# Kernel optimization log

Measured on AMD Instinct MI355X. Metric: run time of the kernel, lower is better.

The kernel has to match this reference:

```python
import jax, jax.numpy as jnp
import numpy as np

DIM_X, H1, H2 = 1024, 2048, 512
SL, SU = 8192, 16384
K_TRIES = 8  # vectorized stand-in for the per-sample rejection-sampling while-loop


def setup_inputs() -> dict:
    key = jax.random.key(0)
    ks = jax.random.split(key, 10)
    s = 0.02
    return {
        "X_l": jax.random.normal(ks[0], (SL, DIM_X), jnp.float32),
        "y_l": jax.random.normal(ks[1], (SL,), jnp.float32),
        "X_u": jax.random.normal(ks[2], (SU, DIM_X), jnp.float32),
        "y_u": jax.random.normal(ks[3], (SU,), jnp.float32),
        "W1": jax.random.normal(ks[4], (DIM_X, H1), jnp.float32) * s,
        "b1": jnp.zeros((H1,), jnp.float32),
        "W2": jax.random.normal(ks[5], (H1, H2), jnp.float32) * s,
        "b2": jnp.zeros((H2,), jnp.float32),
        "W3": jax.random.normal(ks[6], (H2, 1), jnp.float32) * s,
        "b3": jnp.zeros((1,), jnp.float32),
    }


def _sample_pairs(key, y_l, size_u):
    """For each unlabeled sample, draw a labeled pair (a, b) with a != b and
    y_l[a] != y_l[b] (mirrors torch.randperm + rejection loop). K candidate
    draws per sample; first valid candidate is taken (valid w.h.p. for
    continuous y_l)."""
    size_l = y_l.shape[0]
    ka, kb = jax.random.split(key)
    ia = jax.random.randint(ka, (size_u, K_TRIES), 0, size_l)  # [SU, K]
    ib = jax.random.randint(kb, (size_u, K_TRIES), 0, size_l)
    valid = (ia != ib) & (y_l[ia] != y_l[ib])
    first = jnp.argmax(valid, axis=1)  # first valid candidate per row
    a = jnp.take_along_axis(ia, first[:, None], axis=1)[:, 0]
    b = jnp.take_along_axis(ib, first[:, None], axis=1)[:, 0]
    return a, b


def reference(X_l, y_l, X_u, y_u, W1, b1, W2, b2, W3, b3):
    def encode(x):
        h = jax.nn.relu(x @ W1 + b1)
        return jax.nn.relu(h @ W2 + b2)

    feat_l = encode(X_l)          # [SL, H2]
    feat_u = encode(X_u)          # [SU, H2]
    y_hat = feat_l @ W3 + b3      # [SL, 1]

    a, b = _sample_pairs(jax.random.key(42), y_l, X_u.shape[0])
    k = (y_u - y_l[b]) / (y_l[a] - y_l[b])            # [SU]
    feat_comb = k[:, None] * feat_l[a] + (1.0 - k)[:, None] * feat_l[b]
    return feat_u, feat_comb, y_hat
```

## Files before the change

kernel.cpp:

```cpp
#include <hip/hip_runtime.h>
#include <stdint.h>

#define SLAB 8192
#define SUNL 16384
#define DIMX 1024
#define HID1 2048
#define HID2 512
#define KTRIES 8
#define MTOT (SLAB + SUNL)

typedef __attribute__((ext_vector_type(8))) short bf16x8;
typedef __attribute__((ext_vector_type(4))) float f32x4;

__device__ __forceinline__ unsigned short f2bf(float f) {
  union { float f; uint32_t u; } c; c.f = f;
  return (unsigned short)((c.u + 0x7fffu + ((c.u >> 16) & 1u)) >> 16);
}

__device__ __forceinline__ void async16(const void* g, void* l) {
  __builtin_amdgcn_global_load_lds(
      (const __attribute__((address_space(1))) unsigned int*)g,
      (__attribute__((address_space(3))) unsigned int*)l,
      16, 0, 0);
}

struct U2 { uint32_t x, y; };

__device__ __forceinline__ U2 threefry(uint32_t k0, uint32_t k1, uint32_t x0, uint32_t x1) {
  uint32_t ks2 = k0 ^ k1 ^ 0x1BD11BDAu;
  x0 += k0; x1 += k1;
#define TF_R(r) { x0 += x1; x1 = (x1 << (r)) | (x1 >> (32 - (r))); x1 ^= x0; }
  TF_R(13) TF_R(15) TF_R(26) TF_R(6)
  x0 += k1; x1 += ks2 + 1u;
  TF_R(17) TF_R(29) TF_R(16) TF_R(24)
  x0 += ks2; x1 += k0 + 2u;
  TF_R(13) TF_R(15) TF_R(26) TF_R(6)
  x0 += k0; x1 += k1 + 3u;
  TF_R(17) TF_R(29) TF_R(16) TF_R(24)
  x0 += k1; x1 += ks2 + 4u;
  TF_R(13) TF_R(15) TF_R(26) TF_R(6)
  x0 += ks2; x1 += k0 + 5u;
#undef TF_R
  return {x0, x1};
}

#define XL_BLOCKS (SLAB * DIMX / 4 / 256)
#define CAST_BLOCKS (MTOT * DIMX / 4 / 256)
#define T1_NBX (HID1 / 32)
#define T1_BLOCKS ((HID1 / 32) * (DIMX / 32))
#define T2_NBX (HID2 / 32)
#define T2_BLOCKS ((HID2 / 32) * (HID1 / 32))
#define PAIR_BLOCKS (SUNL / 256)
#define PREP_BLOCKS (CAST_BLOCKS + T1_BLOCKS + T2_BLOCKS + PAIR_BLOCKS)

__global__ __launch_bounds__(256) void prep_kernel(
    const float* __restrict__ Xl, const float* __restrict__ Xu,
    const float* __restrict__ W1, const float* __restrict__ W2,
    const float* __restrict__ y_l, const float* __restrict__ y_u,
    unsigned short* __restrict__ X_bf, unsigned short* __restrict__ W1T,
    unsigned short* __restrict__ W2T,
    int* __restrict__ ia, int* __restrict__ ib, float* __restrict__ kv)
{
  __shared__ float t[32][33];
  int b = blockIdx.x;
  int tid = threadIdx.x;

  if (b < CAST_BLOCKS) {
    const float* src; size_t i, doff;
    if (b < XL_BLOCKS) { src = Xl; i = (size_t)b * 256 + tid; doff = 0; }
    else { src = Xu; i = (size_t)(b - XL_BLOCKS) * 256 + tid; doff = (size_t)SLAB * DIMX / 4; }
    float4 v = ((const float4*)src)[i];
    ushort4 o;
    o.x = f2bf(v.x); o.y = f2bf(v.y); o.z = f2bf(v.z); o.w = f2bf(v.w);
    ((ushort4*)X_bf)[doff + i] = o;
  } else if (b < CAST_BLOCKS + T1_BLOCKS + T2_BLOCKS) {
    const float* W; unsigned short* WT; int K, N, bx, by;
    if (b < CAST_BLOCKS + T1_BLOCKS) {
      int tb = b - CAST_BLOCKS;
      W = W1; WT = W1T; K = DIMX; N = HID1; bx = tb % T1_NBX; by = tb / T1_NBX;
    } else {
      int tb = b - CAST_BLOCKS - T1_BLOCKS;
      W = W2; WT = W2T; K = HID1; N = HID2; bx = tb % T2_NBX; by = tb / T2_NBX;
    }
    int k0 = by * 32, n0 = bx * 32;
    int tx = tid & 31, ty = tid >> 5;
#pragma unroll
    for (int i = 0; i < 32; i += 8)
      t[ty + i][tx] = W[(size_t)(k0 + ty + i) * N + n0 + tx];
    __syncthreads();
#pragma unroll
    for (int i = 0; i < 32; i += 8)
      WT[(size_t)(n0 + ty + i) * K + k0 + tx] = f2bf(t[tx][ty + i]);
  } else {
    int r = (b - CAST_BLOCKS - T1_BLOCKS - T2_BLOCKS) * 256 + tid;
    U2 ka  = threefry(0u, 42u, 0u, 0u);
    U2 kb  = threefry(0u, 42u, 0u, 1u);
    U2 k2a = threefry(ka.x, ka.y, 0u, 1u);
    U2 k2b = threefry(kb.x, kb.y, 0u, 1u);
    int iav[KTRIES], ibv[KTRIES];
#pragma unroll
    for (int c = 0; c < KTRIES; ++c) {
      uint32_t tt = (uint32_t)(r * KTRIES + c);
      U2 oa = threefry(k2a.x, k2a.y, 0u, tt);
      U2 ob = threefry(k2b.x, k2b.y, 0u, tt);
      iav[c] = (int)((oa.x ^ oa.y) & (SLAB - 1));
      ibv[c] = (int)((ob.x ^ ob.y) & (SLAB - 1));
    }
    int a = iav[0], bb2 = ibv[0];
#pragma unroll
    for (int c = 0; c < KTRIES; ++c) {
      if (iav[c] != ibv[c] && y_l[iav[c]] != y_l[ibv[c]]) { a = iav[c]; bb2 = ibv[c]; break; }
    }
    float ya = y_l[a], yb = y_l[bb2];
    ia[r] = a; ib[r] = bb2; kv[r] = (y_u[r] - yb) / (ya - yb);
  }
}

#define GROUP_M 8
#define MFMA_B16(a, b, c) __builtin_amdgcn_mfma_f32_16x16x32_bf16(a, b, c, 0, 0, 0)
#define SBAR __builtin_amdgcn_sched_barrier(0)

template<bool QP, bool ST, int VMC, bool BARS, bool PRE>
__device__ __forceinline__ void ktile32(
    const unsigned short* AsB, const unsigned short* BsB,
    unsigned short* AsS, unsigned short* BsS,
    const unsigned short* AsN, const unsigned short* BsN,
    const unsigned short* gA0, const unsigned short* gA1,
    const unsigned short* gB0, const unsigned short* gB1,
    int kk2, int ldstA, int ofsA, int ofsB,
    bf16x8 (&ha0)[4], bf16x8 (&hb0)[2],
    bf16x8 (&na0)[4], bf16x8 (&nb0)[2],
    bf16x8 (&ca1)[4], bf16x8 (&cb1)[2],
    bf16x8 (&ta1)[4], bf16x8 (&tb1)[2],
    f32x4 (&acc)[8][4])
{
#pragma unroll
  for (int j = 0; j < 2; ++j)
    tb1[j] = *(const bf16x8*)(BsB + ofsB + (j + 2) * 512);
  SBAR;
  if (QP) {
    __builtin_amdgcn_s_setprio(1);
#pragma unroll
    for (int i = 0; i < 4; ++i)
#pragma unroll
      for (int j = 0; j < 2; ++j)
        acc[i + 4][j + 2] = MFMA_B16(ca1[i], cb1[j], acc[i + 4][j + 2]);
    __builtin_amdgcn_s_setprio(0);
    SBAR;
  }
  asm volatile("s_waitcnt lgkmcnt(2)" ::: "memory");
  SBAR;
  __builtin_amdgcn_s_setprio(1);
#pragma unroll
  for (int i = 0; i < 4; ++i)
#pragma unroll
    for (int j = 0; j < 2; ++j)
      acc[i][j] = MFMA_B16(ha0[i], hb0[j], acc[i][j]);
  __builtin_amdgcn_s_setprio(0);
  SBAR;

#pragma unroll
  for (int i = 0; i < 4; ++i)
    ta1[i] = *(const bf16x8*)(AsB + ofsA + (i + 4) * 512);
  SBAR;
  asm volatile("s_waitcnt lgkmcnt(4)" ::: "memory");
  SBAR;
  __builtin_amdgcn_s_setprio(1);
#pragma unroll
  for (int i = 0; i < 4; ++i)
#pragma unroll
    for (int j = 0; j < 2; ++j)
      acc[i][j + 2] = MFMA_B16(ha0[i], tb1[j], acc[i][j + 2]);
  __builtin_amdgcn_s_setprio(0);
  asm volatile("s_waitcnt lgkmcnt(0)" ::: "memory");
  SBAR;
  if (BARS) __builtin_amdgcn_s_barrier();

  if (ST) {
    async16(gA0 + kk2, AsS + ldstA);
    async16(gA1 + kk2, AsS + 4096 + ldstA);
    async16(gB0 + kk2, BsS + ldstA);
    async16(gB1 + kk2, BsS + 4096 + ldstA);
    SBAR;
  }
  __builtin_amdgcn_s_setprio(1);
#pragma unroll
  for (int i = 0; i < 4; ++i)
#pragma unroll
    for (int j = 0; j < 2; ++j)
      acc[i + 4][j] = MFMA_B16(ta1[i], hb0[j], acc[i + 4][j]);
  __builtin_amdgcn_s_setprio(0);
  if (VMC == 4)      asm volatile("s_waitcnt vmcnt(4)" ::: "memory");
  else if (VMC == 0) asm volatile("s_waitcnt vmcnt(0)" ::: "memory");
  if (BARS) __builtin_amdgcn_s_barrier();

  if (PRE) {
#pragma unroll
    for (int i = 0; i < 4; ++i)
      na0[i] = *(const bf16x8*)(AsN + ofsA + i * 512);
#pragma unroll
    for (int j = 0; j < 2; ++j)
      nb0[j] = *(const bf16x8*)(BsN + ofsB + j * 512);
    SBAR;
  }
}

template<int OUT_BF16, int RELU>
__global__ __launch_bounds__(512, 2) void gemm_bt_256(
    const unsigned short* __restrict__ A,
    const unsigned short* __restrict__ Bt,
    const float* __restrict__ bias,
    void* __restrict__ C0, void* __restrict__ C1, int Msplit,
    int M, int N, int K)
{
  __shared__ unsigned short As[2][8192];
  __shared__ unsigned short Bs[2][8192];

  const int tid  = threadIdx.x;
  const int wave = tid >> 6;
  const int lane = tid & 63;

  const int nbx = N >> 8;
  const int gsize = nbx * GROUP_M;
  const int grp = blockIdx.x / gsize, within = blockIdx.x % gsize;
  const int m0 = (grp * GROUP_M + (within % GROUP_M)) << 8;
  const int n0 = (within / GROUP_M) << 8;

  const int wm = (wave >> 2) << 7;
  const int wn = (wave & 3) << 6;

  const int srow   = tid >> 2;
  const int schunk = (tid & 3) ^ ((srow >> 1) & 3);
  const unsigned short* gA0 = A  + (size_t)(m0 + srow) * K + schunk * 8;
  const unsigned short* gA1 = gA0 + (size_t)128 * K;
  const unsigned short* gB0 = Bt + (size_t)(n0 + srow) * K + schunk * 8;
  const unsigned short* gB1 = gB0 + (size_t)128 * K;
  const int ldstA = wave << 9;

  const int fr = lane & 15, q = lane >> 4;
  const int cs = (q ^ ((fr >> 1) & 3)) << 3;
  const int ofsA = ((wm + fr) << 5) + cs;
  const int ofsB = ((wn + fr) << 5) + cs;

  f32x4 acc[8][4] = {};
  bf16x8 a0A[4], b0A[2], a0B[4], b0B[2];
  bf16x8 a1A[4], b1A[2], a1B[4], b1B[2];

  unsigned short* A0p = &As[0][0]; unsigned short* B0p = &Bs[0][0];
  unsigned short* A1p = &As[1][0]; unsigned short* B1p = &Bs[1][0];

  async16(gA0,      A0p + ldstA);
  async16(gA1,      A0p + 4096 + ldstA);
  async16(gB0,      B0p + ldstA);
  async16(gB1,      B0p + 4096 + ldstA);
  async16(gA0 + 32, A1p + ldstA);
  async16(gA1 + 32, A1p + 4096 + ldstA);
  async16(gB0 + 32, B1p + ldstA);
  async16(gB1 + 32, B1p + 4096 + ldstA);
  asm volatile("s_waitcnt vmcnt(4)" ::: "memory");
  __builtin_amdgcn_s_barrier();
#pragma unroll
  for (int i = 0; i < 4; ++i)
    a0A[i] = *(const bf16x8*)(A0p + ofsA + i * 512);
#pragma unroll
  for (int j = 0; j < 2; ++j)
    b0A[j] = *(const bf16x8*)(B0p + ofsB + j * 512);
  SBAR;

  const int NT = K >> 5;

  ktile32<false, true, 4, true, true>(A0p, B0p, A0p, B0p, A1p, B1p,
      gA0, gA1, gB0, gB1, 2 * 32, ldstA, ofsA, ofsB,
      a0A, b0A, a0B, b0B, a1B, b1B, a1A, b1A, acc);
#pragma unroll 1
  for (int t = 1; t <= NT - 5; t += 2) {
    ktile32<true, true, 4, true, true>(A1p, B1p, A1p, B1p, A0p, B0p,
        gA0, gA1, gB0, gB1, (t + 2) * 32, ldstA, ofsA, ofsB,
        a0B, b0B, a0A, b0A, a1A, b1A, a1B, b1B, acc);
    ktile32<true, true, 4, true, true>(A0p, B0p, A0p, B0p, A1p, B1p,
        gA0, gA1, gB0, gB1, (t + 3) * 32, ldstA, ofsA, ofsB,
        a0A, b0A, a0B, b0B, a1B, b1B, a1A, b1A, acc);
  }
  ktile32<true, true, 4, true, true>(A1p, B1p, A1p, B1p, A0p, B0p,
      gA0, gA1, gB0, gB1, (NT - 1) * 32, ldstA, ofsA, ofsB,
      a0B, b0B, a0A, b0A, a1A, b1A, a1B, b1B, acc);
  ktile32<true, false, 0, true, true>(A0p, B0p, A0p, B0p, A1p, B1p,
      gA0, gA1, gB0, gB1, 0, ldstA, ofsA, ofsB,
      a0A, b0A, a0B, b0B, a1B, b1B, a1A, b1A, acc);
  ktile32<true, false, -1, false, false>(A1p, B1p, A1p, B1p, A0p, B0p,
      gA0, gA1, gB0, gB1, 0, ldstA, ofsA, ofsB,
      a0B, b0B, a0A, b0A, a1A, b1A, a1B, b1B, acc);
  __builtin_amdgcn_s_setprio(1);
#pragma unroll
  for (int i = 0; i < 4; ++i)
#pragma unroll
    for (int j = 0; j < 2; ++j)
      acc[i + 4][j + 2] = MFMA_B16(a1B[i], b1B[j], acc[i + 4][j + 2]);
  __builtin_amdgcn_s_setprio(0);

  void* Cb = (m0 < Msplit) ? C0 : C1;
  const int mbase = (m0 < Msplit) ? m0 : (m0 - Msplit);
  const int crow = mbase + wm + (lane >> 4) * 4;
  const int ccol = n0 + wn + (lane & 15);
  float bv[4];
#pragma unroll
  for (int j = 0; j < 4; ++j) bv[j] = bias[ccol + j * 16];
#pragma unroll
  for (int i = 0; i < 8; ++i) {
#pragma unroll
    for (int r = 0; r < 4; ++r) {
      size_t base = (size_t)(crow + i * 16 + r) * N + ccol;
#pragma unroll
      for (int j = 0; j < 4; ++j) {
        float v = acc[i][j][r] + bv[j];
        if (RELU) v = fmaxf(v, 0.0f);
        if (OUT_BF16) ((unsigned short*)Cb)[base + j * 16] = f2bf(v);
        else          ((float*)Cb)[base + j * 16] = v;
      }
    }
  }
}

#define COMB_BLOCKS (SUNL / 2)
#define YHAT_BLOCKS (SLAB / 4)
#define POST_BLOCKS (COMB_BLOCKS + YHAT_BLOCKS)

__global__ __launch_bounds__(256) void post_kernel(
    const float* __restrict__ feat_l, const float* __restrict__ W3,
    const float* __restrict__ b3, const int* __restrict__ ia,
    const int* __restrict__ ib, const float* __restrict__ kv,
    float* __restrict__ out_comb, float* __restrict__ out_yhat)
{
  int b = blockIdx.x;
  if (b < COMB_BLOCKS) {
    int row = b * 2 + (threadIdx.x >> 7);
    int c = (threadIdx.x & 127) << 2;
    float k = kv[row];
    float km1 = 1.0f - k;
    float4 fa = *(const float4*)(feat_l + (size_t)ia[row] * HID2 + c);
    float4 fb = *(const float4*)(feat_l + (size_t)ib[row] * HID2 + c);
    float4 o;
    o.x = k * fa.x + km1 * fb.x;
    o.y = k * fa.y + km1 * fb.y;
    o.z = k * fa.z + km1 * fb.z;
    o.w = k * fa.w + km1 * fb.w;
    *(float4*)(out_comb + (size_t)row * HID2 + c) = o;
  } else {
    int wave = threadIdx.x >> 6;
    int lane = threadIdx.x & 63;
    int row = (b - COMB_BLOCKS) * 4 + wave;
    const float* f = feat_l + (size_t)row * HID2;
    float s = 0.f;
#pragma unroll
    for (int j = 0; j < HID2 / 64; ++j) s = fmaf(f[lane + j * 64], W3[lane + j * 64], s);
#pragma unroll
    for (int off = 32; off; off >>= 1) s += __shfl_down(s, off);
    if (lane == 0) out_yhat[row] = s + b3[0];
  }
}

extern "C" void kernel_launch(void* const* d_in, const int* in_sizes, int n_in,
                              void* d_out, int out_size, void* d_ws, size_t ws_size,
                              hipStream_t stream)
{
  const float* X_l = (const float*)d_in[0];
  const float* y_l = (const float*)d_in[1];
  const float* X_u = (const float*)d_in[2];
  const float* y_u = (const float*)d_in[3];
  const float* W1  = (const float*)d_in[4];
  const float* b1  = (const float*)d_in[5];
  const float* W2  = (const float*)d_in[6];
  const float* b2  = (const float*)d_in[7];
  const float* W3  = (const float*)d_in[8];
  const float* b3  = (const float*)d_in[9];

  float* out_featu = (float*)d_out;
  float* out_comb  = out_featu + (size_t)SUNL * HID2;
  float* out_yhat  = out_comb + (size_t)SUNL * HID2;

  unsigned short* X_bf  = (unsigned short*)d_ws;
  unsigned short* W1T   = X_bf + (size_t)MTOT * DIMX;
  unsigned short* W2T   = W1T + (size_t)HID1 * DIMX;
  unsigned short* H_bf  = W2T + (size_t)HID2 * HID1;
  float* feat_l = (float*)(H_bf + (size_t)MTOT * HID1);
  int*   ai = (int*)(feat_l + (size_t)SLAB * HID2);
  int*   bi = ai + SUNL;
  float* kv = (float*)(bi + SUNL);

  prep_kernel<<<dim3(PREP_BLOCKS), dim3(256), 0, stream>>>(
      X_l, X_u, W1, W2, y_l, y_u, X_bf, W1T, W2T, ai, bi, kv);

  gemm_bt_256<1, 1><<<dim3((HID1 / 256) * (MTOT / 256)), dim3(512), 0, stream>>>(
      X_bf, W1T, b1, H_bf, H_bf, MTOT , MTOT, HID1, DIMX);

  gemm_bt_256<0, 1><<<dim3((HID2 / 256) * (MTOT / 256)), dim3(512), 0, stream>>>(
      H_bf, W2T, b2, feat_l, out_featu, SLAB, MTOT, HID2, HID1);

  post_kernel<<<dim3(POST_BLOCKS), dim3(256), 0, stream>>>(
      feat_l, W3, b3, ai, bi, kv, out_comb, out_yhat);
}
```

Baseline: 333.0 us.

## Double K-tile depth to 64 per LDS stage with barrier-free inner sub-step

Each LDS buffer now holds a 64-wide K slice instead of 32, with a new 8-chunk XOR swizzle and row stride of 64 elements. Every stage is processed as two 32-wide sub-steps, and only the second sub-step issues global-to-LDS loads and block barriers. This halves the number of barriers and waitcnt synchronisations per unit of K. In exchange LDS use doubles to 128 KB per block, which may limit occupancy at the requested two blocks per CU.

```diff
diff --git a/kernel.cpp b/kernel.cpp
--- a/kernel.cpp
+++ b/kernel.cpp
@@ -120,14 +120,14 @@
 #define MFMA_B16(a, b, c) __builtin_amdgcn_mfma_f32_16x16x32_bf16(a, b, c, 0, 0, 0)
 #define SBAR __builtin_amdgcn_sched_barrier(0)
 
-template<bool QP, bool ST, int VMC, bool BARS, bool PRE>
-__device__ __forceinline__ void ktile32(
+template<bool QP, bool BARS, bool ST, int VMC, bool PRE>
+__device__ __forceinline__ void ksub(
     const unsigned short* AsB, const unsigned short* BsB,
     unsigned short* AsS, unsigned short* BsS,
-    const unsigned short* AsN, const unsigned short* BsN,
-    const unsigned short* gA0, const unsigned short* gA1,
-    const unsigned short* gB0, const unsigned short* gB1,
-    int kk2, int ldstA, int ofsA, int ofsB,
+    const unsigned short* AsP, const unsigned short* BsP,
+    const unsigned short* gA, const unsigned short* gB,
+    int kk2, int K, int ldst,
+    int ofsA, int ofsB, int ofsAp, int ofsBp,
     bf16x8 (&ha0)[4], bf16x8 (&hb0)[2],
     bf16x8 (&na0)[4], bf16x8 (&nb0)[2],
     bf16x8 (&ca1)[4], bf16x8 (&cb1)[2],
@@ -136,7 +136,7 @@
 {
 #pragma unroll
   for (int j = 0; j < 2; ++j)
-    tb1[j] = *(const bf16x8*)(BsB + ofsB + (j + 2) * 512);
+    tb1[j] = *(const bf16x8*)(BsB + ofsB + (j + 2) * 1024);
   SBAR;
   if (QP) {
     __builtin_amdgcn_s_setprio(1);
@@ -161,7 +161,7 @@
 
 #pragma unroll
   for (int i = 0; i < 4; ++i)
-    ta1[i] = *(const bf16x8*)(AsB + ofsA + (i + 4) * 512);
+    ta1[i] = *(const bf16x8*)(AsB + ofsA + (i + 4) * 1024);
   SBAR;
   asm volatile("s_waitcnt lgkmcnt(4)" ::: "memory");
   SBAR;
@@ -175,12 +175,12 @@
   asm volatile("s_waitcnt lgkmcnt(0)" ::: "memory");
   SBAR;
   if (BARS) __builtin_amdgcn_s_barrier();
-
   if (ST) {
-    async16(gA0 + kk2, AsS + ldstA);
-    async16(gA1 + kk2, AsS + 4096 + ldstA);
-    async16(gB0 + kk2, BsS + ldstA);
-    async16(gB1 + kk2, BsS + 4096 + ldstA);
+#pragma unroll
+    for (int c = 0; c < 4; ++c) {
+      async16(gA + (size_t)(c * 64) * K + kk2, AsS + c * 4096 + ldst);
+      async16(gB + (size_t)(c * 64) * K + kk2, BsS + c * 4096 + ldst);
+    }
     SBAR;
   }
   __builtin_amdgcn_s_setprio(1);
@@ -190,17 +190,17 @@
     for (int j = 0; j < 2; ++j)
       acc[i + 4][j] = MFMA_B16(ta1[i], hb0[j], acc[i + 4][j]);
   __builtin_amdgcn_s_setprio(0);
-  if (VMC == 4)      asm volatile("s_waitcnt vmcnt(4)" ::: "memory");
+  if (VMC == 8)      asm volatile("s_waitcnt vmcnt(8)" ::: "memory");
   else if (VMC == 0) asm volatile("s_waitcnt vmcnt(0)" ::: "memory");
   if (BARS) __builtin_amdgcn_s_barrier();
 
   if (PRE) {
 #pragma unroll
     for (int i = 0; i < 4; ++i)
-      na0[i] = *(const bf16x8*)(AsN + ofsA + i * 512);
+      na0[i] = *(const bf16x8*)(AsP + ofsAp + i * 1024);
 #pragma unroll
     for (int j = 0; j < 2; ++j)
-      nb0[j] = *(const bf16x8*)(BsN + ofsB + j * 512);
+      nb0[j] = *(const bf16x8*)(BsP + ofsBp + j * 1024);
     SBAR;
   }
 }
@@ -213,8 +213,8 @@
     void* __restrict__ C0, void* __restrict__ C1, int Msplit,
     int M, int N, int K)
 {
-  __shared__ unsigned short As[2][8192];
-  __shared__ unsigned short Bs[2][8192];
+  __shared__ unsigned short As[2][16384];
+  __shared__ unsigned short Bs[2][16384];
 
   const int tid  = threadIdx.x;
   const int wave = tid >> 6;
@@ -229,18 +229,18 @@
   const int wm = (wave >> 2) << 7;
   const int wn = (wave & 3) << 6;
 
-  const int srow   = tid >> 2;
-  const int schunk = (tid & 3) ^ ((srow >> 1) & 3);
-  const unsigned short* gA0 = A  + (size_t)(m0 + srow) * K + schunk * 8;
-  const unsigned short* gA1 = gA0 + (size_t)128 * K;
-  const unsigned short* gB0 = Bt + (size_t)(n0 + srow) * K + schunk * 8;
-  const unsigned short* gB1 = gB0 + (size_t)128 * K;
-  const int ldstA = wave << 9;
+  const int srow   = tid >> 3;
+  const int schunk = (tid & 7) ^ (srow & 7);
+  const unsigned short* gA = A  + (size_t)(m0 + srow) * K + schunk * 8;
+  const unsigned short* gB = Bt + (size_t)(n0 + srow) * K + schunk * 8;
+  const int ldst = wave << 9;
 
   const int fr = lane & 15, q = lane >> 4;
-  const int cs = (q ^ ((fr >> 1) & 3)) << 3;
-  const int ofsA = ((wm + fr) << 5) + cs;
-  const int ofsB = ((wn + fr) << 5) + cs;
+  const int cs0 = (q ^ (fr & 7)) << 3;
+  const int ofsA0 = ((wm + fr) << 6) + cs0;
+  const int ofsB0 = ((wn + fr) << 6) + cs0;
+  const int ofsA1 = ofsA0 ^ 32;
+  const int ofsB1 = ofsB0 ^ 32;
 
   f32x4 acc[8][4] = {};
   bf16x8 a0A[4], b0A[2], a0B[4], b0B[2];
@@ -249,46 +249,67 @@
   unsigned short* A0p = &As[0][0]; unsigned short* B0p = &Bs[0][0];
   unsigned short* A1p = &As[1][0]; unsigned short* B1p = &Bs[1][0];
 
-  async16(gA0,      A0p + ldstA);
-  async16(gA1,      A0p + 4096 + ldstA);
-  async16(gB0,      B0p + ldstA);
-  async16(gB1,      B0p + 4096 + ldstA);
-  async16(gA0 + 32, A1p + ldstA);
-  async16(gA1 + 32, A1p + 4096 + ldstA);
-  async16(gB0 + 32, B1p + ldstA);
-  async16(gB1 + 32, B1p + 4096 + ldstA);
-  asm volatile("s_waitcnt vmcnt(4)" ::: "memory");
+#pragma unroll
+  for (int c = 0; c < 4; ++c) {
+    async16(gA + (size_t)(c * 64) * K,      A0p + c * 4096 + ldst);
+    async16(gB + (size_t)(c * 64) * K,      B0p + c * 4096 + ldst);
+  }
+#pragma unroll
+  for (int c = 0; c < 4; ++c) {
+    async16(gA + (size_t)(c * 64) * K + 64, A1p + c * 4096 + ldst);
+    async16(gB + (size_t)(c * 64) * K + 64, B1p + c * 4096 + ldst);
+  }
+  asm volatile("s_waitcnt vmcnt(8)" ::: "memory");
   __builtin_amdgcn_s_barrier();
 #pragma unroll
   for (int i = 0; i < 4; ++i)
-    a0A[i] = *(const bf16x8*)(A0p + ofsA + i * 512);
+    a0A[i] = *(const bf16x8*)(A0p + ofsA0 + i * 1024);
 #pragma unroll
   for (int j = 0; j < 2; ++j)
-    b0A[j] = *(const bf16x8*)(B0p + ofsB + j * 512);
-  SBAR;
-
-  const int NT = K >> 5;
-
-  ktile32<false, true, 4, true, true>(A0p, B0p, A0p, B0p, A1p, B1p,
-      gA0, gA1, gB0, gB1, 2 * 32, ldstA, ofsA, ofsB,
+    b0A[j] = *(const bf16x8*)(B0p + ofsB0 + j * 1024);
+  SBAR;
+
+  const int NT = K >> 6;
+
+  ksub<false, false, false, -1, true>(A0p, B0p, A0p, B0p, A0p, B0p, gA, gB,
+      0, K, ldst, ofsA0, ofsB0, ofsA1, ofsB1,
       a0A, b0A, a0B, b0B, a1B, b1B, a1A, b1A, acc);
+  ksub<true, true, true, 8, true>(A0p, B0p, A0p, B0p, A1p, B1p, gA, gB,
+      2 * 64, K, ldst, ofsA1, ofsB1, ofsA0, ofsB0,
+      a0B, b0B, a0A, b0A, a1A, b1A, a1B, b1B, acc);
+
 #pragma unroll 1
-  for (int t = 1; t <= NT - 5; t += 2) {
-    ktile32<true, true, 4, true, true>(A1p, B1p, A1p, B1p, A0p, B0p,
-        gA0, gA1, gB0, gB1, (t + 2) * 32, ldstA, ofsA, ofsB,
+  for (int t = 1; t <= NT - 4; t += 2) {
+    ksub<true, false, false, -1, true>(A1p, B1p, A1p, B1p, A1p, B1p, gA, gB,
+        0, K, ldst, ofsA0, ofsB0, ofsA1, ofsB1,
+        a0A, b0A, a0B, b0B, a1B, b1B, a1A, b1A, acc);
+    ksub<true, true, true, 8, true>(A1p, B1p, A1p, B1p, A0p, B0p, gA, gB,
+        (t + 2) * 64, K, ldst, ofsA1, ofsB1, ofsA0, ofsB0,
         a0B, b0B, a0A, b0A, a1A, b1A, a1B, b1B, acc);
-    ktile32<true, true, 4, true, true>(A0p, B0p, A0p, B0p, A1p, B1p,
-        gA0, gA1, gB0, gB1, (t + 3) * 32, ldstA, ofsA, ofsB,
+    ksub<true, false, false, -1, true>(A0p, B0p, A0p, B0p, A0p, B0p, gA, gB,
+        0, K, ldst, ofsA0, ofsB0, ofsA1, ofsB1,
         a0A, b0A, a0B, b0B, a1B, b1B, a1A, b1A, acc);
-  }
-  ktile32<true, true, 4, true, true>(A1p, B1p, A1p, B1p, A0p, B0p,
-      gA0, gA1, gB0, gB1, (NT - 1) * 32, ldstA, ofsA, ofsB,
+    ksub<true, true, true, 8, true>(A0p, B0p, A0p, B0p, A1p, B1p, gA, gB,
+        (t + 3) * 64, K, ldst, ofsA1, ofsB1, ofsA0, ofsB0,
+        a0B, b0B, a0A, b0A, a1A, b1A, a1B, b1B, acc);
+  }
+  ksub<true, false, false, -1, true>(A1p, B1p, A1p, B1p, A1p, B1p, gA, gB,
+      0, K, ldst, ofsA0, ofsB0, ofsA1, ofsB1,
+      a0A, b0A, a0B, b0B, a1B, b1B, a1A, b1A, acc);
+  ksub<true, true, true, 8, true>(A1p, B1p, A1p, B1p, A0p, B0p, gA, gB,
+      (NT - 1) * 64, K, ldst, ofsA1, ofsB1, ofsA0, ofsB0,
       a0B, b0B, a0A, b0A, a1A, b1A, a1B, b1B, acc);
-  ktile32<true, false, 0, true, true>(A0p, B0p, A0p, B0p, A1p, B1p,
-      gA0, gA1, gB0, gB1, 0, ldstA, ofsA, ofsB,
+  ksub<true, false, false, -1, true>(A0p, B0p, A0p, B0p, A0p, B0p, gA, gB,
+      0, K, ldst, ofsA0, ofsB0, ofsA1, ofsB1,
       a0A, b0A, a0B, b0B, a1B, b1B, a1A, b1A, acc);
-  ktile32<true, false, -1, false, false>(A1p, B1p, A1p, B1p, A0p, B0p,
-      gA0, gA1, gB0, gB1, 0, ldstA, ofsA, ofsB,
+  ksub<true, true, false, 0, true>(A0p, B0p, A0p, B0p, A1p, B1p, gA, gB,
+      0, K, ldst, ofsA1, ofsB1, ofsA0, ofsB0,
+      a0B, b0B, a0A, b0A, a1A, b1A, a1B, b1B, acc);
+  ksub<true, false, false, -1, true>(A1p, B1p, A1p, B1p, A1p, B1p, gA, gB,
+      0, K, ldst, ofsA0, ofsB0, ofsA1, ofsB1,
+      a0A, b0A, a0B, b0B, a1B, b1B, a1A, b1A, acc);
+  ksub<true, false, false, -1, false>(A1p, B1p, A1p, B1p, A1p, B1p, gA, gB,
+      0, K, ldst, ofsA1, ofsB1, ofsA0, ofsB0,
       a0B, b0B, a0A, b0A, a1A, b1A, a1B, b1B, acc);
   __builtin_amdgcn_s_setprio(1);
 #pragma unroll
```

Measured after the change: 329.7 us. About the same (-1.0%).

## Shrink GEMM block tile to 128x256 with four waves

Applied to the files above, without the earlier changes.

Both encoder GEMMs now use 128x256 output tiles computed by 256-thread blocks instead of 256x256 tiles with 512 threads. Each wave covers 64x128, and the LDS staging and wait counts are reworked to match the new load pattern. The grid doubles, which is meant to improve load balance across CUs, especially for the narrow second GEMM (N=512). In exchange, each block reuses A less per loaded B tile and issues more global loads per unit of output.

```diff
diff --git a/kernel.cpp b/kernel.cpp
--- a/kernel.cpp
+++ b/kernel.cpp
@@ -121,99 +121,98 @@
 #define SBAR __builtin_amdgcn_sched_barrier(0)
 
 template<bool QP, bool ST, int VMC, bool BARS, bool PRE>
-__device__ __forceinline__ void ktile32(
+__device__ __forceinline__ void ksub(
     const unsigned short* AsB, const unsigned short* BsB,
     unsigned short* AsS, unsigned short* BsS,
-    const unsigned short* AsN, const unsigned short* BsN,
-    const unsigned short* gA0, const unsigned short* gA1,
-    const unsigned short* gB0, const unsigned short* gB1,
-    int kk2, int ldstA, int ofsA, int ofsB,
-    bf16x8 (&ha0)[4], bf16x8 (&hb0)[2],
-    bf16x8 (&na0)[4], bf16x8 (&nb0)[2],
-    bf16x8 (&ca1)[4], bf16x8 (&cb1)[2],
-    bf16x8 (&ta1)[4], bf16x8 (&tb1)[2],
-    f32x4 (&acc)[8][4])
+    const unsigned short* AsP, const unsigned short* BsP,
+    const unsigned short* gA, const unsigned short* gB,
+    int kk2, int K, int ldst, int ofsA, int ofsB,
+    bf16x8 (&ha0)[2], bf16x8 (&hb0)[4],
+    bf16x8 (&na0)[2], bf16x8 (&nb0)[4],
+    bf16x8 (&ca1)[2], bf16x8 (&cb1)[4],
+    bf16x8 (&ta1)[2], bf16x8 (&tb1)[4],
+    f32x4 (&acc)[4][8])
 {
 #pragma unroll
-  for (int j = 0; j < 2; ++j)
-    tb1[j] = *(const bf16x8*)(BsB + ofsB + (j + 2) * 512);
+  for (int j = 0; j < 4; ++j)
+    tb1[j] = *(const bf16x8*)(BsB + ofsB + (j + 4) * 512);
   SBAR;
   if (QP) {
     __builtin_amdgcn_s_setprio(1);
 #pragma unroll
-    for (int i = 0; i < 4; ++i)
-#pragma unroll
-      for (int j = 0; j < 2; ++j)
-        acc[i + 4][j + 2] = MFMA_B16(ca1[i], cb1[j], acc[i + 4][j + 2]);
+    for (int i = 0; i < 2; ++i)
+#pragma unroll
+      for (int j = 0; j < 4; ++j)
+        acc[i + 2][j + 4] = MFMA_B16(ca1[i], cb1[j], acc[i + 2][j + 4]);
     __builtin_amdgcn_s_setprio(0);
     SBAR;
   }
-  asm volatile("s_waitcnt lgkmcnt(2)" ::: "memory");
+  asm volatile("s_waitcnt lgkmcnt(4)" ::: "memory");
   SBAR;
   __builtin_amdgcn_s_setprio(1);
 #pragma unroll
-  for (int i = 0; i < 4; ++i)
-#pragma unroll
-    for (int j = 0; j < 2; ++j)
+  for (int i = 0; i < 2; ++i)
+#pragma unroll
+    for (int j = 0; j < 4; ++j)
       acc[i][j] = MFMA_B16(ha0[i], hb0[j], acc[i][j]);
   __builtin_amdgcn_s_setprio(0);
   SBAR;
 
 #pragma unroll
-  for (int i = 0; i < 4; ++i)
-    ta1[i] = *(const bf16x8*)(AsB + ofsA + (i + 4) * 512);
-  SBAR;
-  asm volatile("s_waitcnt lgkmcnt(4)" ::: "memory");
+  for (int i = 0; i < 2; ++i)
+    ta1[i] = *(const bf16x8*)(AsB + ofsA + (i + 2) * 512);
+  SBAR;
+  asm volatile("s_waitcnt lgkmcnt(2)" ::: "memory");
   SBAR;
   __builtin_amdgcn_s_setprio(1);
 #pragma unroll
-  for (int i = 0; i < 4; ++i)
-#pragma unroll
-    for (int j = 0; j < 2; ++j)
-      acc[i][j + 2] = MFMA_B16(ha0[i], tb1[j], acc[i][j + 2]);
+  for (int i = 0; i < 2; ++i)
+#pragma unroll
+    for (int j = 0; j < 4; ++j)
+      acc[i][j + 4] = MFMA_B16(ha0[i], tb1[j], acc[i][j + 4]);
   __builtin_amdgcn_s_setprio(0);
   asm volatile("s_waitcnt lgkmcnt(0)" ::: "memory");
   SBAR;
   if (BARS) __builtin_amdgcn_s_barrier();
-
   if (ST) {
-    async16(gA0 + kk2, AsS + ldstA);
-    async16(gA1 + kk2, AsS + 4096 + ldstA);
-    async16(gB0 + kk2, BsS + ldstA);
-    async16(gB1 + kk2, BsS + 4096 + ldstA);
+    async16(gA + kk2,                  AsS + ldst);
+    async16(gA + (size_t)64 * K + kk2, AsS + 2048 + ldst);
+#pragma unroll
+    for (int c = 0; c < 4; ++c)
+      async16(gB + (size_t)(c * 64) * K + kk2, BsS + c * 2048 + ldst);
     SBAR;
   }
   __builtin_amdgcn_s_setprio(1);
 #pragma unroll
-  for (int i = 0; i < 4; ++i)
-#pragma unroll
-    for (int j = 0; j < 2; ++j)
-      acc[i + 4][j] = MFMA_B16(ta1[i], hb0[j], acc[i + 4][j]);
+  for (int i = 0; i < 2; ++i)
+#pragma unroll
+    for (int j = 0; j < 4; ++j)
+      acc[i + 2][j] = MFMA_B16(ta1[i], hb0[j], acc[i + 2][j]);
   __builtin_amdgcn_s_setprio(0);
-  if (VMC == 4)      asm volatile("s_waitcnt vmcnt(4)" ::: "memory");
+  if (VMC == 6)      asm volatile("s_waitcnt vmcnt(6)" ::: "memory");
   else if (VMC == 0) asm volatile("s_waitcnt vmcnt(0)" ::: "memory");
   if (BARS) __builtin_amdgcn_s_barrier();
 
   if (PRE) {
 #pragma unroll
-    for (int i = 0; i < 4; ++i)
-      na0[i] = *(const bf16x8*)(AsN + ofsA + i * 512);
-#pragma unroll
-    for (int j = 0; j < 2; ++j)
-      nb0[j] = *(const bf16x8*)(BsN + ofsB + j * 512);
+    for (int i = 0; i < 2; ++i)
+      na0[i] = *(const bf16x8*)(AsP + ofsA + i * 512);
+#pragma unroll
+    for (int j = 0; j < 4; ++j)
+      nb0[j] = *(const bf16x8*)(BsP + ofsB + j * 512);
     SBAR;
   }
 }
 
 template<int OUT_BF16, int RELU>
-__global__ __launch_bounds__(512, 2) void gemm_bt_256(
+__global__ __launch_bounds__(256, 2) void gemm_bt_128(
     const unsigned short* __restrict__ A,
     const unsigned short* __restrict__ Bt,
     const float* __restrict__ bias,
     void* __restrict__ C0, void* __restrict__ C1, int Msplit,
     int M, int N, int K)
 {
-  __shared__ unsigned short As[2][8192];
+  __shared__ unsigned short As[2][4096];
   __shared__ unsigned short Bs[2][8192];
 
   const int tid  = threadIdx.x;
@@ -223,95 +222,95 @@
   const int nbx = N >> 8;
   const int gsize = nbx * GROUP_M;
   const int grp = blockIdx.x / gsize, within = blockIdx.x % gsize;
-  const int m0 = (grp * GROUP_M + (within % GROUP_M)) << 8;
+  const int m0 = (grp * GROUP_M + (within % GROUP_M)) << 7;
   const int n0 = (within / GROUP_M) << 8;
 
-  const int wm = (wave >> 2) << 7;
-  const int wn = (wave & 3) << 6;
+  const int wm = (wave >> 1) << 6;
+  const int wn = (wave & 1) << 7;
 
   const int srow   = tid >> 2;
   const int schunk = (tid & 3) ^ ((srow >> 1) & 3);
-  const unsigned short* gA0 = A  + (size_t)(m0 + srow) * K + schunk * 8;
-  const unsigned short* gA1 = gA0 + (size_t)128 * K;
-  const unsigned short* gB0 = Bt + (size_t)(n0 + srow) * K + schunk * 8;
-  const unsigned short* gB1 = gB0 + (size_t)128 * K;
-  const int ldstA = wave << 9;
+  const unsigned short* gA = A  + (size_t)(m0 + srow) * K + schunk * 8;
+  const unsigned short* gB = Bt + (size_t)(n0 + srow) * K + schunk * 8;
+  const int ldst = wave << 9;
 
   const int fr = lane & 15, q = lane >> 4;
   const int cs = (q ^ ((fr >> 1) & 3)) << 3;
   const int ofsA = ((wm + fr) << 5) + cs;
   const int ofsB = ((wn + fr) << 5) + cs;
 
-  f32x4 acc[8][4] = {};
-  bf16x8 a0A[4], b0A[2], a0B[4], b0B[2];
-  bf16x8 a1A[4], b1A[2], a1B[4], b1B[2];
+  f32x4 acc[4][8] = {};
+  bf16x8 a0A[2], b0A[4], a0B[2], b0B[4];
+  bf16x8 a1A[2], b1A[4], a1B[2], b1B[4];
 
   unsigned short* A0p = &As[0][0]; unsigned short* B0p = &Bs[0][0];
   unsigned short* A1p = &As[1][0]; unsigned short* B1p = &Bs[1][0];
 
-  async16(gA0,      A0p + ldstA);
-  async16(gA1,      A0p + 4096 + ldstA);
-  async16(gB0,      B0p + ldstA);
-  async16(gB1,      B0p + 4096 + ldstA);
-  async16(gA0 + 32, A1p + ldstA);
-  async16(gA1 + 32, A1p + 4096 + ldstA);
-  async16(gB0 + 32, B1p + ldstA);
-  async16(gB1 + 32, B1p + 4096 + ldstA);
-  asm volatile("s_waitcnt vmcnt(4)" ::: "memory");
+  async16(gA,                  A0p + ldst);
+  async16(gA + (size_t)64 * K, A0p + 2048 + ldst);
+#pragma unroll
+  for (int c = 0; c < 4; ++c)
+    async16(gB + (size_t)(c * 64) * K,      B0p + c * 2048 + ldst);
+  async16(gA + 32,                  A1p + ldst);
+  async16(gA + (size_t)64 * K + 32, A1p + 2048 + ldst);
+#pragma unroll
+  for (int c = 0; c < 4; ++c)
+    async16(gB + (size_t)(c * 64) * K + 32, B1p + c * 2048 + ldst);
+  asm volatile("s_waitcnt vmcnt(6)" ::: "memory");
   __builtin_amdgcn_s_barrier();
 #pragma unroll
-  for (int i = 0; i < 4; ++i)
+  for (int i = 0; i < 2; ++i)
     a0A[i] = *(const bf16x8*)(A0p + ofsA + i * 512);
 #pragma unroll
-  for (int j = 0; j < 2; ++j)
+  for (int j = 0; j < 4; ++j)
     b0A[j] = *(const bf16x8*)(B0p + ofsB + j * 512);
   SBAR;
 
   const int NT = K >> 5;
 
-  ktile32<false, true, 4, true, true>(A0p, B0p, A0p, B0p, A1p, B1p,
-      gA0, gA1, gB0, gB1, 2 * 32, ldstA, ofsA, ofsB,
+  ksub<false, true, 6, true, true>(A0p, B0p, A0p, B0p, A1p, B1p, gA, gB,
+      2 * 32, K, ldst, ofsA, ofsB,
       a0A, b0A, a0B, b0B, a1B, b1B, a1A, b1A, acc);
 #pragma unroll 1
   for (int t = 1; t <= NT - 5; t += 2) {
-    ktile32<true, true, 4, true, true>(A1p, B1p, A1p, B1p, A0p, B0p,
-        gA0, gA1, gB0, gB1, (t + 2) * 32, ldstA, ofsA, ofsB,
+    ksub<true, true, 6, true, true>(A1p, B1p, A1p, B1p, A0p, B0p, gA, gB,
+        (t + 2) * 32, K, ldst, ofsA, ofsB,
         a0B, b0B, a0A, b0A, a1A, b1A, a1B, b1B, acc);
-    ktile32<true, true, 4, true, true>(A0p, B0p, A0p, B0p, A1p, B1p,
-        gA0, gA1, gB0, gB1, (t + 3) * 32, ldstA, ofsA, ofsB,
+    ksub<true, true, 6, true, true>(A0p, B0p, A0p, B0p, A1p, B1p, gA, gB,
+        (t + 3) * 32, K, ldst, ofsA, ofsB,
         a0A, b0A, a0B, b0B, a1B, b1B, a1A, b1A, acc);
   }
-  ktile32<true, true, 4, true, true>(A1p, B1p, A1p, B1p, A0p, B0p,
-      gA0, gA1, gB0, gB1, (NT - 1) * 32, ldstA, ofsA, ofsB,
+  ksub<true, true, 6, true, true>(A1p, B1p, A1p, B1p, A0p, B0p, gA, gB,
+      (NT - 1) * 32, K, ldst, ofsA, ofsB,
       a0B, b0B, a0A, b0A, a1A, b1A, a1B, b1B, acc);
-  ktile32<true, false, 0, true, true>(A0p, B0p, A0p, B0p, A1p, B1p,
-      gA0, gA1, gB0, gB1, 0, ldstA, ofsA, ofsB,
+  ksub<true, false, 0, true, true>(A0p, B0p, A0p, B0p, A1p, B1p, gA, gB,
+      0, K, ldst, ofsA, ofsB,
       a0A, b0A, a0B, b0B, a1B, b1B, a1A, b1A, acc);
-  ktile32<true, false, -1, false, false>(A1p, B1p, A1p, B1p, A0p, B0p,
-      gA0, gA1, gB0, gB1, 0, ldstA, ofsA, ofsB,
+  ksub<true, false, -1, false, false>(A1p, B1p, A1p, B1p, A0p, B0p, gA, gB,
+      0, K, ldst, ofsA, ofsB,
       a0B, b0B, a0A, b0A, a1A, b1A, a1B, b1B, acc);
   __builtin_amdgcn_s_setprio(1);
 #pragma unroll
-  for (int i = 0; i < 4; ++i)
-#pragma unroll
-    for (int j = 0; j < 2; ++j)
-      acc[i + 4][j + 2] = MFMA_B16(a1B[i], b1B[j], acc[i + 4][j + 2]);
+  for (int i = 0; i < 2; ++i)
+#pragma unroll
+    for (int j = 0; j < 4; ++j)
+      acc[i + 2][j + 4] = MFMA_B16(a1B[i], b1B[j], acc[i + 2][j + 4]);
   __builtin_amdgcn_s_setprio(0);
 
   void* Cb = (m0 < Msplit) ? C0 : C1;
   const int mbase = (m0 < Msplit) ? m0 : (m0 - Msplit);
   const int crow = mbase + wm + (lane >> 4) * 4;
   const int ccol = n0 + wn + (lane & 15);
-  float bv[4];
-#pragma unroll
-  for (int j = 0; j < 4; ++j) bv[j] = bias[ccol + j * 16];
-#pragma unroll
-  for (int i = 0; i < 8; ++i) {
+  float bv[8];
+#pragma unroll
+  for (int j = 0; j < 8; ++j) bv[j] = bias[ccol + j * 16];
+#pragma unroll
+  for (int i = 0; i < 4; ++i) {
 #pragma unroll
     for (int r = 0; r < 4; ++r) {
       size_t base = (size_t)(crow + i * 16 + r) * N + ccol;
 #pragma unroll
-      for (int j = 0; j < 4; ++j) {
+      for (int j = 0; j < 8; ++j) {
         float v = acc[i][j][r] + bv[j];
         if (RELU) v = fmaxf(v, 0.0f);
         if (OUT_BF16) ((unsigned short*)Cb)[base + j * 16] = f2bf(v);
@@ -390,10 +389,10 @@
   prep_kernel<<<dim3(PREP_BLOCKS), dim3(256), 0, stream>>>(
       X_l, X_u, W1, W2, y_l, y_u, X_bf, W1T, W2T, ai, bi, kv);
 
-  gemm_bt_256<1, 1><<<dim3((HID1 / 256) * (MTOT / 256)), dim3(512), 0, stream>>>(
+  gemm_bt_128<1, 1><<<dim3((HID1 / 256) * (MTOT / 128)), dim3(256), 0, stream>>>(
       X_bf, W1T, b1, H_bf, H_bf, MTOT , MTOT, HID1, DIMX);
 
-  gemm_bt_256<0, 1><<<dim3((HID2 / 256) * (MTOT / 256)), dim3(512), 0, stream>>>(
+  gemm_bt_128<0, 1><<<dim3((HID2 / 256) * (MTOT / 128)), dim3(256), 0, stream>>>(
       H_bf, W2T, b2, feat_l, out_featu, SLAB, MTOT, HID2, HID1);
 
   post_kernel<<<dim3(POST_BLOCKS), dim3(256), 0, stream>>>(
```

Measured after the change: 349.6 us. 5.0% more time.
